# Kernel tuning notes

Measured on AMD Instinct MI355X. Metric: run time of the kernel, lower is better.

Reference implementation:

```python
import jax, jax.numpy as jnp
import numpy as np


def setup_inputs() -> dict:
    key = jax.random.key(0)
    ks = jax.random.split(key, 6)
    nt, ne, b, vs = 48, 48, 32, 512
    targets = jax.random.normal(ks[0], (nt, b, vs), dtype=jnp.float32)
    embeddings = jax.random.normal(ks[1], (ne, b, vs), dtype=jnp.float32)
    # torch nn.Linear(2*dim, dim): weight [dim, 2*dim], bias [dim]
    W1 = jax.random.normal(ks[2], (vs, 2 * vs), dtype=jnp.float32) * (1.0 / np.sqrt(2 * vs))
    b1 = jax.random.normal(ks[3], (vs,), dtype=jnp.float32) * 0.01
    # nn.Linear(dim, 1): weight [1, dim], bias [1]
    W2 = jax.random.normal(ks[4], (1, vs), dtype=jnp.float32) * (1.0 / np.sqrt(vs))
    b2 = jax.random.normal(ks[5], (1,), dtype=jnp.float32) * 0.01
    return {"targets": targets, "embeddings": embeddings, "W1": W1, "b1": b1, "W2": W2, "b2": b2}


def reference(targets, embeddings, W1, b1, W2, b2):
    # targets: [nt, b, vs], embeddings: [ne, b, vs]
    # Original: cat(expand(targets), expand(embeddings), dim=3) @ W1^T.
    # Because concat feeds a linear layer, split W1 = [W1a | W1b] and compute
    # the two matmuls on the small tensors, then broadcast-add — same math,
    # no [nt, ne, b, 2*vs] intermediate.
    vs = targets.shape[-1]
    W1a = W1[:, :vs]   # acts on targets half
    W1b = W1[:, vs:]   # acts on embeddings half
    ta = jnp.einsum('tbv,hv->tbh', targets, W1a)      # [nt, b, dim]
    eb = jnp.einsum('nbv,hv->nbh', embeddings, W1b)   # [ne, b, dim]
    h = jnp.tanh(ta[:, None] + eb[None, :] + b1)       # [nt, ne, b, dim]
    out = jnp.einsum('tnbh,h->tnb', h, W2[0]) + b2[0]  # [nt, ne, b]
    return out
```

## Files before the change

### kernel.cpp

```cpp
#include <hip/hip_runtime.h>
#include <hip/hip_bf16.h>

typedef float f32x4 __attribute__((ext_vector_type(4)));
typedef short s16x8 __attribute__((ext_vector_type(8)));

#define NT 48
#define NE 48
#define NB 32
#define VS 512
#define NOUT (NT * NE * NB)
#define CX_OFF (3072 * 512)

__global__ __launch_bounds__(256) void k_gemm(
    const float* __restrict__ targets, const float* __restrict__ embeddings,
    const float* __restrict__ W1, const float* __restrict__ b1,
    const float* __restrict__ W2, const float* __restrict__ b2,
    float* __restrict__ C, float* __restrict__ out) {
  __shared__ short sa[2][64][40];
  __shared__ short sb[2][64][40];

  const int bid = blockIdx.x;
  const int tid = threadIdx.x;

  {
    int zi = bid * 256 + tid;
    if (zi < NOUT) out[zi] = 0.0f;
  }
  if (bid == 0 && tid < 64) {
#pragma unroll
    for (int q = 0; q < 4; ++q) {
      float s = W2[q * 128 + tid] + W2[q * 128 + 64 + tid];
#pragma unroll
      for (int off = 32; off; off >>= 1) s += __shfl_xor(s, off, 64);
      if (tid == 0) C[CX_OFF + q] = 0.25f * b2[0] + s;
    }
  }

  const int mt = bid >> 3;
  const int ht = bid & 7;
  const int m0 = mt * 64, h0 = ht * 64;
  const bool is_ta = (m0 < 1536);
  const float* Abase = is_ta ? (targets + (size_t)m0 * VS)
                             : (embeddings + (size_t)(m0 - 1536) * VS);
  const float* Bbase = W1 + (size_t)h0 * 1024 + (is_ta ? 0 : 512);

  const int lane = tid & 63, w = tid >> 6;
  const int q = lane >> 4, i = lane & 15;

  const float* gsrc[4];
  int loff[4];
  bool isA[4];
#pragma unroll
  for (int r = 0; r < 4; ++r) {
    int f = r * 256 + tid;
    int g = f & 511;
    int row = g >> 3;
    int col4 = (g & 7) << 2;
    isA[r] = (f < 512);
    gsrc[r] = isA[r] ? (Abase + (size_t)row * VS + col4)
                     : (Bbase + (size_t)row * 1024 + col4);
    loff[r] = row * 40 + col4;
  }

  f32x4 acc[4] = {{0.f,0.f,0.f,0.f},{0.f,0.f,0.f,0.f},{0.f,0.f,0.f,0.f},{0.f,0.f,0.f,0.f}};

  f32x4 v[4];
#pragma unroll
  for (int r = 0; r < 4; ++r) v[r] = *(const f32x4*)(gsrc[r]);

  for (int kt = 0; kt < 16; ++kt) {
    const int p = kt & 1;
#pragma unroll
    for (int r = 0; r < 4; ++r) {
      union { __hip_bfloat162 h2; unsigned u; } c0, c1;
      c0.h2 = __float22bfloat162_rn(float2{v[r][0], v[r][1]});
      c1.h2 = __float22bfloat162_rn(float2{v[r][2], v[r][3]});
      uint2 o; o.x = c0.u; o.y = c1.u;
      short* base = isA[r] ? &sa[p][0][0] : &sb[p][0][0];
      *(uint2*)(base + loff[r]) = o;
    }
    __syncthreads();
    if (kt < 15) {
      const int k1 = (kt + 1) * 32;
#pragma unroll
      for (int r = 0; r < 4; ++r) v[r] = *(const f32x4*)(gsrc[r] + k1);
    }
    s16x8 av = *(const s16x8*)&sa[p][16 * w + i][q * 8];
#pragma unroll
    for (int c = 0; c < 4; ++c) {
      s16x8 bv = *(const s16x8*)&sb[p][c * 16 + i][q * 8];
      acc[c] = __builtin_amdgcn_mfma_f32_16x16x32_bf16(av, bv, acc[c], 0, 0, 0);
    }
  }

#pragma unroll
  for (int c = 0; c < 4; ++c) {
#pragma unroll
    for (int r = 0; r < 4; ++r) {
      int ml = 16 * w + q * 4 + r;
      int hl = c * 16 + i;
      int m = m0 + ml, h = h0 + hl;
      float vv = acc[c][r];
      if (is_ta) vv += b1[h];
      C[(size_t)m * VS + h] = __expf(vv + vv);
    }
  }
}

__global__ __launch_bounds__(512) void k_fuse(
    const float* __restrict__ C, const float* __restrict__ W2,
    float* __restrict__ out) {
  __shared__ float sta[16][132];
  __shared__ float seb[16][132];
  __shared__ float w2c[128];
  __shared__ float red[8][16][17];

  const int bid = blockIdx.x;
  const int b = bid & 31;
  const int r5 = bid >> 5;
  const int hq = r5 & 3;
  const int r2 = r5 >> 2;
  const int t0 = (r2 / 3) * 16, n0 = (r2 % 3) * 16;

  const int tid = threadIdx.x;

#pragma unroll
  for (int rr = 0; rr < 2; ++rr) {
    int f = rr * 512 + tid;
    int g = f & 511;
    int row = g >> 5;
    int col4 = (g & 31) << 2;
    int m = (f < 512) ? ((t0 + row) * NB + b)
                      : (1536 + (n0 + row) * NB + b);
    f32x4 v = *(const f32x4*)&C[(size_t)m * VS + hq * 128 + col4];
    float* dst = (f < 512) ? &sta[row][col4] : &seb[row][col4];
    *(f32x4*)dst = v;
  }
  if (tid < 32) *(f32x4*)&w2c[tid * 4] = *(const f32x4*)&W2[hq * 128 + tid * 4];
  __syncthreads();

  const int w = tid >> 6, lane = tid & 63;
  const int i0 = lane & 7, j0 = (lane >> 3) & 7;
  const int hb = w * 16;

  float a00 = 0.f, a01 = 0.f, a10 = 0.f, a11 = 0.f;
#pragma unroll
  for (int it = 0; it < 4; ++it) {
    int h = hb + it * 4;
    f32x4 et0 = *(const f32x4*)&sta[i0][h];
    f32x4 et1 = *(const f32x4*)&sta[i0 + 8][h];
    f32x4 en0 = *(const f32x4*)&seb[j0][h];
    f32x4 en1 = *(const f32x4*)&seb[j0 + 8][h];
    f32x4 w4  = *(const f32x4*)&w2c[h];
#pragma unroll
    for (int u = 0; u < 4; ++u) {
      float r00 = __builtin_amdgcn_rcpf(et0[u] * en0[u] + 1.0f);
      float r01 = __builtin_amdgcn_rcpf(et0[u] * en1[u] + 1.0f);
      float r10 = __builtin_amdgcn_rcpf(et1[u] * en0[u] + 1.0f);
      float r11 = __builtin_amdgcn_rcpf(et1[u] * en1[u] + 1.0f);
      float ww = w4[u];
      a00 += ww * r00; a01 += ww * r01; a10 += ww * r10; a11 += ww * r11;
    }
  }

  red[w][i0][j0]         = a00;
  red[w][i0][j0 + 8]     = a01;
  red[w][i0 + 8][j0]     = a10;
  red[w][i0 + 8][j0 + 8] = a11;
  __syncthreads();

  if (tid < 256) {
    int tl = tid & 15, nl = tid >> 4;
    float s = 0.f;
#pragma unroll
    for (int ww = 0; ww < 8; ++ww) s += red[ww][tl][nl];
    float val = C[CX_OFF + hq] - 2.0f * s;
    atomicAdd(&out[((size_t)(t0 + tl) * NE + (n0 + nl)) * NB + b], val);
  }
}

extern "C" void kernel_launch(void* const* d_in, const int* in_sizes, int n_in,
                              void* d_out, int out_size, void* d_ws, size_t ws_size,
                              hipStream_t stream) {
  (void)in_sizes; (void)n_in; (void)out_size; (void)ws_size;
  const float* targets    = (const float*)d_in[0];
  const float* embeddings = (const float*)d_in[1];
  const float* W1         = (const float*)d_in[2];
  const float* b1         = (const float*)d_in[3];
  const float* W2         = (const float*)d_in[4];
  const float* b2         = (const float*)d_in[5];
  float* out = (float*)d_out;
  float* C   = (float*)d_ws;

  k_gemm<<<dim3(384), dim3(256), 0, stream>>>(targets, embeddings, W1, b1, W2, b2, C, out);
  k_fuse<<<dim3(1152), dim3(512), 0, stream>>>(C, W2, out);
}
```

Measured before the change: 100.9 us.

## Restructure fuse kernel with transposed LDS tiles and 4x4 register blocking

The fuse kernel now runs 256 threads per block instead of 512. Each thread computes a 4x4 (t,n) tile over a strided subset of h, reading from LDS tiles that are stored h-major (transposed) with padded rows. The cross-thread reduction is rewritten to reuse the same shared memory, with an XOR swizzle to avoid bank conflicts, and only 64 threads finish the sum. The goal is more register reuse and fewer LDS loads per rcp/FMA. The cost is scalar strided global loads during the transpose-on-load and a longer final reduction done by fewer threads.

```diff
diff --git a/kernel.cpp b/kernel.cpp
--- a/kernel.cpp
+++ b/kernel.cpp
@@ -107,75 +107,96 @@
   }
 }
 
-__global__ __launch_bounds__(512) void k_fuse(
+#define ETS 20
+#define RPS 20
+__global__ __launch_bounds__(256) void k_fuse(
     const float* __restrict__ C, const float* __restrict__ W2,
     float* __restrict__ out) {
-  __shared__ float sta[16][132];
-  __shared__ float seb[16][132];
-  __shared__ float w2c[128];
-  __shared__ float red[8][16][17];
+  __shared__ float smem[128 * ETS * 2 + 128];
+  float* etT = smem;
+  float* enT = smem + 128 * ETS;
+  float* w2c = smem + 256 * ETS;
+  float* red = smem;
 
   const int bid = blockIdx.x;
-  const int b = bid & 31;
+  const int b  = bid & 31;
   const int r5 = bid >> 5;
   const int hq = r5 & 3;
   const int r2 = r5 >> 2;
   const int t0 = (r2 / 3) * 16, n0 = (r2 % 3) * 16;
-
   const int tid = threadIdx.x;
 
 #pragma unroll
-  for (int rr = 0; rr < 2; ++rr) {
-    int f = rr * 512 + tid;
-    int g = f & 511;
-    int row = g >> 5;
-    int col4 = (g & 31) << 2;
-    int m = (f < 512) ? ((t0 + row) * NB + b)
-                      : (1536 + (n0 + row) * NB + b);
-    f32x4 v = *(const f32x4*)&C[(size_t)m * VS + hq * 128 + col4];
-    float* dst = (f < 512) ? &sta[row][col4] : &seb[row][col4];
+  for (int r = 0; r < 4; ++r) {
+    int z = r * 256 + tid;
+    int c2 = z & 511;
+    int q  = c2 >> 7;
+    int h  = c2 & 127;
+    bool isE = (z >= 512);
+    f32x4 v;
+#pragma unroll
+    for (int rr = 0; rr < 4; ++rr) {
+      int row = q * 4 + rr;
+      int m = isE ? (1536 + (n0 + row) * NB + b) : ((t0 + row) * NB + b);
+      v[rr] = C[(size_t)m * VS + hq * 128 + h];
+    }
+    float* dst = (isE ? enT : etT) + h * ETS + q * 4;
     *(f32x4*)dst = v;
   }
   if (tid < 32) *(f32x4*)&w2c[tid * 4] = *(const f32x4*)&W2[hq * 128 + tid * 4];
   __syncthreads();
 
-  const int w = tid >> 6, lane = tid & 63;
-  const int i0 = lane & 7, j0 = (lane >> 3) & 7;
-  const int hb = w * 16;
-
-  float a00 = 0.f, a01 = 0.f, a10 = 0.f, a11 = 0.f;
-#pragma unroll
-  for (int it = 0; it < 4; ++it) {
-    int h = hb + it * 4;
-    f32x4 et0 = *(const f32x4*)&sta[i0][h];
-    f32x4 et1 = *(const f32x4*)&sta[i0 + 8][h];
-    f32x4 en0 = *(const f32x4*)&seb[j0][h];
-    f32x4 en1 = *(const f32x4*)&seb[j0 + 8][h];
-    f32x4 w4  = *(const f32x4*)&w2c[h];
+  const int w    = tid >> 6;
+  const int lane = tid & 63;
+  const int pn   = lane >> 4;
+  const int hsub = lane & 15;
+
+  float w2v[8];
+#pragma unroll
+  for (int s = 0; s < 8; ++s) w2v[s] = w2c[hsub + 16 * s];
+
+  float acc[4][4] = {{0.f,0.f,0.f,0.f},{0.f,0.f,0.f,0.f},{0.f,0.f,0.f,0.f},{0.f,0.f,0.f,0.f}};
+#pragma unroll
+  for (int s = 0; s < 8; ++s) {
+    int h = hsub + 16 * s;
+    f32x4 et = *(const f32x4*)&etT[h * ETS + w * 4];
+    f32x4 en = *(const f32x4*)&enT[h * ETS + pn * 4];
+    float ww = w2v[s];
+#pragma unroll
+    for (int r = 0; r < 4; ++r)
+#pragma unroll
+      for (int u = 0; u < 4; ++u) {
+        float rc = __builtin_amdgcn_rcpf(et[r] * en[u] + 1.0f);
+        acc[r][u] += ww * rc;
+      }
+  }
+  __syncthreads();
+
+  {
+    float* dst = &red[((hsub * 16) + (w * 4 + pn)) * RPS];
+#pragma unroll
+    for (int r = 0; r < 4; ++r) {
+      f32x4 v = { acc[r][0], acc[r][1], acc[r][2], acc[r][3] };
+      *(f32x4*)&dst[(r ^ (hsub & 3)) * 4] = v;
+    }
+  }
+  __syncthreads();
+
+  if (tid < 64) {
+    int i = tid >> 2, jq = tid & 3;
+    int pos = (i >> 2) * 4 + jq;
+    f32x4 ssum = {0.f, 0.f, 0.f, 0.f};
+#pragma unroll
+    for (int hs = 0; hs < 16; ++hs) {
+      f32x4 v = *(const f32x4*)&red[(hs * 16 + pos) * RPS + (((i & 3) ^ (hs & 3)) * 4)];
+      ssum += v;
+    }
+    float base = C[CX_OFF + hq];
 #pragma unroll
     for (int u = 0; u < 4; ++u) {
-      float r00 = __builtin_amdgcn_rcpf(et0[u] * en0[u] + 1.0f);
-      float r01 = __builtin_amdgcn_rcpf(et0[u] * en1[u] + 1.0f);
-      float r10 = __builtin_amdgcn_rcpf(et1[u] * en0[u] + 1.0f);
-      float r11 = __builtin_amdgcn_rcpf(et1[u] * en1[u] + 1.0f);
-      float ww = w4[u];
-      a00 += ww * r00; a01 += ww * r01; a10 += ww * r10; a11 += ww * r11;
-    }
-  }
-
-  red[w][i0][j0]         = a00;
-  red[w][i0][j0 + 8]     = a01;
-  red[w][i0 + 8][j0]     = a10;
-  red[w][i0 + 8][j0 + 8] = a11;
-  __syncthreads();
-
-  if (tid < 256) {
-    int tl = tid & 15, nl = tid >> 4;
-    float s = 0.f;
-#pragma unroll
-    for (int ww = 0; ww < 8; ++ww) s += red[ww][tl][nl];
-    float val = C[CX_OFF + hq] - 2.0f * s;
-    atomicAdd(&out[((size_t)(t0 + tl) * NE + (n0 + nl)) * NB + b], val);
+      atomicAdd(&out[((size_t)(t0 + i) * NE + (n0 + jq * 4 + u)) * NB + b],
+                base - 2.0f * ssum[u]);
+    }
   }
 }
 
@@ -193,5 +214,5 @@
   float* C   = (float*)d_ws;
 
   k_gemm<<<dim3(384), dim3(256), 0, stream>>>(targets, embeddings, W1, b1, W2, b2, C, out);
-  k_fuse<<<dim3(1152), dim3(512), 0, stream>>>(C, W2, out);
+  k_fuse<<<dim3(1152), dim3(256), 0, stream>>>(C, W2, out);
 }
```

Result: no change. 100.2 us (-0.6%).
